# Kernel tuning notes

Hardware: AMD Instinct MI355X
Metric: run time of the kernel (lower is better)

Reference implementation:

```python
import jax, jax.numpy as jnp
import numpy as np

B, L, D, F, E, K = 2, 2048, 1024, 4096, 8, 2


def setup_inputs() -> dict:
    key = jax.random.key(0)
    ks = jax.random.split(key, 8)
    s = 0.02
    return {
        "x": jax.random.normal(ks[0], (B, L, D), dtype=jnp.float32),
        "Wg": jax.random.normal(ks[1], (D, E), dtype=jnp.float32) * s,
        "bg": jnp.zeros((E,), dtype=jnp.float32),
        "W1": jax.random.normal(ks[2], (E, D, F), dtype=jnp.float32) * s,
        "b1": jnp.zeros((E, F), dtype=jnp.float32),
        "W2": jax.random.normal(ks[3], (E, F, D), dtype=jnp.float32) * s,
        "b2": jnp.zeros((E, D), dtype=jnp.float32),
    }


def reference(x, Wg, bg, W1, b1, W2, b2):
    num_experts = Wg.shape[1]
    gate_scores = x @ Wg + bg                                # [B,L,E]
    topk_scores, topk_ids = jax.lax.top_k(gate_scores, K)    # [B,L,K]
    topk_weights = jax.nn.softmax(topk_scores, axis=-1)      # [B,L,K]
    gate_probs = jax.nn.softmax(gate_scores, axis=-1)        # [B,L,E]

    onehot = jax.nn.one_hot(topk_ids, num_experts, dtype=x.dtype)  # [B,L,K,E]
    expert_mask = onehot.sum(axis=2)                         # [B,L,E]
    freq = expert_mask.mean(axis=(0, 1))                     # [E]
    prob_mean = gate_probs.mean(axis=(0, 1))                 # [E]
    load_balance_loss = num_experts * jnp.sum(freq * prob_mean)

    # combine weight per token per expert (0 if expert not selected)
    combine = jnp.sum(onehot * topk_weights[..., None], axis=2)    # [B,L,E]

    # dense dispatch: run every expert FFN on all tokens, weight & combine
    h = jnp.einsum('bld,edf->belf', x, W1) + b1[None, :, None, :]  # [B,E,L,F]
    h = jax.nn.gelu(h, approximate=False)                          # exact GELU (torch default)
    y = jnp.einsum('belf,efd->beld', h, W2) + b2[None, :, None, :] # [B,E,L,D]
    out = jnp.einsum('ble,beld->bld', combine, y)                  # [B,L,D]
    return out, load_balance_loss
```

## Files before the change

kernel.cpp:

```cpp
#include <hip/hip_runtime.h>
#include <hip/hip_bf16.h>
#include <cstdint>
#include <cstddef>

#define B_ 2
#define L_ 2048
#define D_ 1024
#define F_ 4096
#define E_ 8
#define NTOK 4096
#define MAXROWS 9216

typedef __hip_bfloat16 bf16;
typedef __attribute__((ext_vector_type(8))) short short8;
typedef __attribute__((ext_vector_type(4))) float floatx4;

typedef const __attribute__((address_space(1))) uint32_t* gptr_t;
typedef __attribute__((address_space(3))) uint32_t* lptr_t;

__device__ __forceinline__ void async_load16(const bf16* gp, bf16* lp) {
    __builtin_amdgcn_global_load_lds((gptr_t)(const void*)gp, (lptr_t)(void*)lp, 16, 0, 0);
}

__device__ __forceinline__ uint16_t bfbits(bf16 h) {
    union { bf16 b; uint16_t u; } v; v.b = h; return v.u;
}
__device__ __forceinline__ uint32_t pack2(float a, float b) {
    return (uint32_t)bfbits(__float2bfloat16(a)) | ((uint32_t)bfbits(__float2bfloat16(b)) << 16);
}
__device__ __forceinline__ float ublo(uint32_t u){ return __uint_as_float(u << 16); }
__device__ __forceinline__ float ubhi(uint32_t u){ return __uint_as_float(u & 0xffff0000u); }

__global__ __launch_bounds__(256) void gate_kernel(
    const float* __restrict__ x, const float* __restrict__ Wg,
    const float* __restrict__ bg, float* __restrict__ psum_pad,
    uint32_t* __restrict__ top_ids, float* __restrict__ top_w)
{
    __shared__ float psum_l[E_];
    int t = threadIdx.x;
    if (t < E_) psum_l[t] = 0.f;
    __syncthreads();

    int wave = t >> 6, lane = t & 63;
    for (int j = 0; j < 4; ++j) {
        int token = blockIdx.x * 16 + wave * 4 + j;
        const float* xr = x + (size_t)token * D_;

        float acc[E_];
#pragma unroll
        for (int e = 0; e < E_; ++e) acc[e] = 0.f;
        for (int i = 0; i < D_/64; ++i) {
            int d = lane + 64*i;
            float xv = xr[d];
            const float4* wr4 = (const float4*)(Wg + (size_t)d * E_);
            float4 wa = wr4[0], wb = wr4[1];
            acc[0] += xv * wa.x;  acc[1] += xv * wa.y;
            acc[2] += xv * wa.z;  acc[3] += xv * wa.w;
            acc[4] += xv * wb.x;  acc[5] += xv * wb.y;
            acc[6] += xv * wb.z;  acc[7] += xv * wb.w;
        }
#pragma unroll
        for (int off = 32; off >= 1; off >>= 1) {
#pragma unroll
            for (int e = 0; e < E_; ++e) acc[e] += __shfl_xor(acc[e], off, 64);
        }
        if (lane == 0) {
            float s[E_];
#pragma unroll
            for (int e = 0; e < E_; ++e) s[e] = acc[e] + bg[e];
            int i0 = 0;
#pragma unroll
            for (int e = 1; e < E_; ++e) if (s[e] > s[i0]) i0 = e;
            int i1 = -1;
#pragma unroll
            for (int e = 0; e < E_; ++e) {
                if (e == i0) continue;
                if (i1 < 0 || s[e] > s[i1]) i1 = e;
            }
            float e1 = expf(s[i1] - s[i0]);
            float w0 = 1.f / (1.f + e1);
            float w1 = e1 * w0;
            top_ids[token] = (uint32_t)i0 | ((uint32_t)i1 << 8);
            top_w[token]        = w0;
            top_w[NTOK + token] = w1;

            float mx = s[i0], p[E_], sum = 0.f;
#pragma unroll
            for (int e = 0; e < E_; ++e) { p[e] = expf(s[e] - mx); sum += p[e]; }
            float inv = 1.f / sum;
#pragma unroll
            for (int e = 0; e < E_; ++e) atomicAdd(&psum_l[e], p[e] * inv);
        }
    }
    __syncthreads();
    if (t < E_) atomicAdd(&psum_pad[t * 32], psum_l[t]);
}

__global__ __launch_bounds__(256) void compact_kernel(
    const uint32_t* __restrict__ top_ids, const float* __restrict__ top_w,
    int* __restrict__ cnt, int* __restrict__ tok_list, float* __restrict__ w_list,
    int* __restrict__ rowid)
{
    int e = blockIdx.x;
    int t = threadIdx.x, wave = t >> 6, lane = t & 63;
    __shared__ int wcnt[4];
    int base = 0;
    for (int r0 = 0; r0 < NTOK; r0 += 256) {
        int token = r0 + t;
        uint32_t ids = top_ids[token];
        int slot = -1;
        if ((int)(ids & 255u) == e) slot = 0;
        else if ((int)((ids >> 8) & 255u) == e) slot = 1;
        unsigned long long mask = __ballot(slot >= 0);
        int lpos = __popcll(mask & ((1ull << lane) - 1ull));
        if (lane == 0) wcnt[wave] = (int)__popcll(mask);
        __syncthreads();
        int woff = 0, tot = 0;
#pragma unroll
        for (int w2 = 0; w2 < 4; ++w2) { if (w2 < wave) woff += wcnt[w2]; tot += wcnt[w2]; }
        if (slot >= 0) {
            int pos = base + woff + lpos;
            tok_list[e*NTOK + pos] = token;
            w_list[e*NTOK + pos]   = top_w[slot*NTOK + token];
            rowid[slot*NTOK + token] = (e << 13) | pos;
        }
        base += tot;
        __syncthreads();
    }
    if (t == 0) cnt[e] = base;
}

__global__ void finalize_gate_kernel(const int* __restrict__ cnt, const float* __restrict__ psum_pad,
                                     int* __restrict__ off, float* __restrict__ loss_out)
{
    int o = 0; float Ls = 0.f;
    for (int e = 0; e < E_; ++e) {
        off[e] = o;
        o += (cnt[e] + 127) & ~127;
        Ls += (float)cnt[e] * psum_pad[e * 32];
    }
    loss_out[0] = (float)E_ * Ls / ((float)NTOK * (float)NTOK);
}

__global__ __launch_bounds__(256) void transpose_bf16_kernel(
    const float* __restrict__ in, bf16* __restrict__ outp, int R, int C)
{
    int tilesR = R >> 7, tilesC = C >> 6;
    int per = tilesR * tilesC;
    int bx = blockIdx.x;
    int e  = bx / per; int r2 = bx % per;
    int tr = r2 / tilesC, tc = r2 % tilesC;
    int r0 = tr << 7, c0 = tc << 6;
    const float* ip = in  + (size_t)e * R * C;
    bf16*        op = outp + (size_t)e * R * C;

    int t = threadIdx.x;
    int c = (t & 15) * 4;
    int r = (t >> 4) * 8;

    const float* p = ip + (size_t)(r0 + r) * C + c0 + c;
    float4 v[8];
#pragma unroll
    for (int j = 0; j < 8; ++j) v[j] = *(const float4*)(p + (size_t)j * C);
    const float* vf = (const float*)v;

#pragma unroll
    for (int i = 0; i < 4; ++i) {
        uint4 o;
        o.x = pack2(vf[0*4+i], vf[1*4+i]);
        o.y = pack2(vf[2*4+i], vf[3*4+i]);
        o.z = pack2(vf[4*4+i], vf[5*4+i]);
        o.w = pack2(vf[6*4+i], vf[7*4+i]);
        *(uint4*)(op + (size_t)(c0 + c + i) * R + r0 + r) = o;
    }
}

__global__ __launch_bounds__(256) void gather_kernel(
    const float* __restrict__ x, const int* __restrict__ cnt, const int* __restrict__ off,
    const int* __restrict__ tok_list, bf16* __restrict__ Xg)
{
    int bx = blockIdx.x;
    int e  = bx >> 12;
    int i  = bx & 4095;
    if (i >= cnt[e]) return;
    int tok = tok_list[e*NTOK + i];
    size_t row = (size_t)(off[e] + i);
    int t = threadIdx.x;
    float4 v = *(const float4*)(x + (size_t)tok * D_ + t*4);
    uint2 uu;
    uu.x = pack2(v.x, v.y);
    uu.y = pack2(v.z, v.w);
    *(uint2*)(Xg + row * D_ + t*4) = uu;
}

__global__ __launch_bounds__(256) void gemm1_kernel(
    const bf16* __restrict__ Xg, const bf16* __restrict__ W1t,
    const float* __restrict__ b1, const int* __restrict__ cnt,
    const int* __restrict__ off, bf16* __restrict__ H)
{
    int bx = blockIdx.x;
    int e  = bx >> 10;
    int r2 = bx & 1023;
    int mtile = r2 >> 5, ntile = r2 & 31;
    int n = cnt[e];
    if (mtile * 128 >= n) return;
    int row0 = off[e] + mtile * 128;
    int f0 = ntile * 128;

    __shared__ bf16 As[128*64];
    __shared__ bf16 Bs[128*64];

    int t = threadIdx.x;
    int wave = t >> 6, lane = t & 63;
    int wm = wave & 1, wn = wave >> 1;
    int q = lane >> 4, ln = lane & 15;
    int sm = lane >> 3, sc = lane & 7;

    const bf16* Abase = Xg  + (size_t)row0 * D_;
    const bf16* Bbase = W1t + ((size_t)e * F_ + f0) * D_;

    floatx4 acc[4][4];
#pragma unroll
    for (int mt = 0; mt < 4; ++mt)
#pragma unroll
        for (int nt = 0; nt < 4; ++nt) acc[mt][nt] = {0.f, 0.f, 0.f, 0.f};

    for (int kt = 0; kt < D_; kt += 64) {
        __syncthreads();
#pragma unroll
        for (int i = 0; i < 4; ++i) {
            int g = wave*4 + i;
            int m = g*8 + sm;
            int ca = sc ^ (m & 7);
            async_load16(Abase + (size_t)m * D_ + kt + ca*8, &As[g*512]);
            async_load16(Bbase + (size_t)m * D_ + kt + ca*8, &Bs[g*512]);
        }
        __syncthreads();
#pragma unroll
        for (int kk = 0; kk < 2; ++kk) {
            short8 av[4], bv[4];
#pragma unroll
            for (int mt = 0; mt < 4; ++mt) {
                int r = wm*64 + mt*16 + ln;
                int cs = (kk*4 + q) ^ (r & 7);
                av[mt] = *(const short8*)&As[r*64 + cs*8];
            }
#pragma unroll
            for (int nt = 0; nt < 4; ++nt) {
                int r = wn*64 + nt*16 + ln;
                int cs = (kk*4 + q) ^ (r & 7);
                bv[nt] = *(const short8*)&Bs[r*64 + cs*8];
            }
#pragma unroll
            for (int mt = 0; mt < 4; ++mt)
#pragma unroll
                for (int nt = 0; nt < 4; ++nt)
                    acc[mt][nt] = __builtin_amdgcn_mfma_f32_16x16x32_bf16(av[mt], bv[nt], acc[mt][nt], 0, 0, 0);
        }
    }

    const float is2 = 0.70710678118654752f;
#pragma unroll
    for (int nt = 0; nt < 4; ++nt) {
        int f = f0 + wn*64 + nt*16 + ln;
        float b1v = b1[(size_t)e * F_ + f];
#pragma unroll
        for (int mt = 0; mt < 4; ++mt) {
            int rl = wm*64 + mt*16 + q*4;
#pragma unroll
            for (int r = 0; r < 4; ++r) {
                float v = acc[mt][nt][r] + b1v;
                v = 0.5f * v * (1.f + erff(v * is2));
                H[(size_t)(row0 + rl + r) * F_ + f] = __float2bfloat16(v);
            }
        }
    }
}

__global__ __launch_bounds__(256) void gemm2_kernel(
    const bf16* __restrict__ H, const bf16* __restrict__ W2t,
    const float* __restrict__ b2, const int* __restrict__ cnt, const int* __restrict__ off,
    bf16* __restrict__ Y)
{
    int bx = blockIdx.x;
    int e   = bx >> 8;
    int rem = bx & 255;
    int mtile = rem >> 3;
    int ntile = rem & 7;
    int n = cnt[e];
    if (mtile * 128 >= n) return;
    int row0 = off[e] + mtile * 128;
    int d0 = ntile * 128;

    __shared__ bf16 As[128*64];
    __shared__ bf16 Bs[128*64];

    int t = threadIdx.x;
    int wave = t >> 6, lane = t & 63;
    int wm = wave & 1, wn = wave >> 1;
    int q = lane >> 4, ln = lane & 15;
    int sm = lane >> 3, sc = lane & 7;

    const bf16* Abase = H   + (size_t)row0 * F_;
    const bf16* Bbase = W2t + ((size_t)e * D_ + d0) * F_;

    floatx4 acc[4][4];
#pragma unroll
    for (int mt = 0; mt < 4; ++mt)
#pragma unroll
        for (int nt = 0; nt < 4; ++nt) acc[mt][nt] = {0.f, 0.f, 0.f, 0.f};

    for (int kt = 0; kt < F_; kt += 64) {
        __syncthreads();
#pragma unroll
        for (int i = 0; i < 4; ++i) {
            int g = wave*4 + i;
            int m = g*8 + sm;
            int ca = sc ^ (m & 7);
            async_load16(Abase + (size_t)m * F_ + kt + ca*8, &As[g*512]);
            async_load16(Bbase + (size_t)m * F_ + kt + ca*8, &Bs[g*512]);
        }
        __syncthreads();
#pragma unroll
        for (int kk = 0; kk < 2; ++kk) {
            short8 av[4], bv[4];
#pragma unroll
            for (int mt = 0; mt < 4; ++mt) {
                int r = wm*64 + mt*16 + ln;
                int cs = (kk*4 + q) ^ (r & 7);
                av[mt] = *(const short8*)&As[r*64 + cs*8];
            }
#pragma unroll
            for (int nt = 0; nt < 4; ++nt) {
                int r = wn*64 + nt*16 + ln;
                int cs = (kk*4 + q) ^ (r & 7);
                bv[nt] = *(const short8*)&Bs[r*64 + cs*8];
            }
#pragma unroll
            for (int mt = 0; mt < 4; ++mt)
#pragma unroll
                for (int nt = 0; nt < 4; ++nt)
                    acc[mt][nt] = __builtin_amdgcn_mfma_f32_16x16x32_bf16(av[mt], bv[nt], acc[mt][nt], 0, 0, 0);
        }
    }

    float b2v[4];
#pragma unroll
    for (int nt = 0; nt < 4; ++nt)
        b2v[nt] = b2[(size_t)e * D_ + d0 + wn*64 + nt*16 + ln];

#pragma unroll
    for (int mt = 0; mt < 4; ++mt) {
#pragma unroll
        for (int r = 0; r < 4; ++r) {
            int loc = wm*64 + mt*16 + q*4 + r;
            int i = mtile*128 + loc;
            if (i < n) {
                bf16* yp = Y + (size_t)(row0 + loc) * D_ + d0;
#pragma unroll
                for (int nt = 0; nt < 4; ++nt)
                    yp[wn*64 + nt*16 + ln] = __float2bfloat16(acc[mt][nt][r] + b2v[nt]);
            }
        }
    }
}

__global__ __launch_bounds__(256) void combine_kernel(
    const bf16* __restrict__ Y, const int* __restrict__ rowid,
    const float* __restrict__ top_w, const int* __restrict__ off,
    float* __restrict__ out)
{
    int tok = blockIdx.x;
    int t = threadIdx.x;
    int v0 = rowid[tok], v1 = rowid[NTOK + tok];
    float w0 = top_w[tok], w1 = top_w[NTOK + tok];
    size_t r0 = (size_t)(off[v0 >> 13] + (v0 & 8191));
    size_t r1 = (size_t)(off[v1 >> 13] + (v1 & 8191));
    uint2 a = *(const uint2*)(Y + r0 * D_ + t*4);
    uint2 b = *(const uint2*)(Y + r1 * D_ + t*4);
    float4 o;
    o.x = w0 * ublo(a.x) + w1 * ublo(b.x);
    o.y = w0 * ubhi(a.x) + w1 * ubhi(b.x);
    o.z = w0 * ublo(a.y) + w1 * ublo(b.y);
    o.w = w0 * ubhi(a.y) + w1 * ubhi(b.y);
    *(float4*)(out + (size_t)tok * D_ + t*4) = o;
}

extern "C" void kernel_launch(void* const* d_in, const int* in_sizes, int n_in,
                              void* d_out, int out_size, void* d_ws, size_t ws_size,
                              hipStream_t stream)
{
    const float* x  = (const float*)d_in[0];
    const float* Wg = (const float*)d_in[1];
    const float* bg = (const float*)d_in[2];
    const float* W1 = (const float*)d_in[3];
    const float* b1 = (const float*)d_in[4];
    const float* W2 = (const float*)d_in[5];
    const float* b2 = (const float*)d_in[6];
    float* out = (float*)d_out;

    char* ws = (char*)d_ws;
    int*      cnt      = (int*)(ws + 0);
    int*      off      = (int*)(ws + 128);
    float*    psum_pad = (float*)(ws + 1024);
    uint32_t* top_ids  = (uint32_t*)(ws + 8192);
    float*    top_w    = (float*)(ws + 8192 + 16384);
    int*      tok_list = (int*)(ws + 65536);
    float*    w_list   = (float*)(ws + 65536 + 131072);
    int*      rowid    = (int*)(ws + 327680);
    size_t o = 1u << 20;
    bf16*  W1t = (bf16*)(ws + o);  o += (size_t)E_ * D_ * F_ * 2;
    bf16*  W2t = (bf16*)(ws + o);  o += (size_t)E_ * F_ * D_ * 2;
    bf16*  Xg  = (bf16*)(ws + o);  o += (size_t)MAXROWS * D_ * 2;
    bf16*  H   = (bf16*)(ws + o);
    bf16*  Y   = Xg;

    hipMemsetAsync(ws + 1024, 0, 1024, stream);

    transpose_bf16_kernel<<<E_ * 8 * 64, 256, 0, stream>>>(W1, W1t, D_, F_);
    transpose_bf16_kernel<<<E_ * 32 * 16, 256, 0, stream>>>(W2, W2t, F_, D_);

    gate_kernel<<<256, 256, 0, stream>>>(x, Wg, bg, psum_pad, top_ids, top_w);
    compact_kernel<<<E_, 256, 0, stream>>>(top_ids, top_w, cnt, tok_list, w_list, rowid);
    finalize_gate_kernel<<<1, 1, 0, stream>>>(cnt, psum_pad, off, out + (size_t)NTOK * D_);
    gather_kernel<<<E_ * 4096, 256, 0, stream>>>(x, cnt, off, tok_list, Xg);

    gemm1_kernel<<<E_ * 32 * 32, 256, 0, stream>>>(Xg, W1t, b1, cnt, off, H);
    gemm2_kernel<<<E_ * 32 * 8, 256, 0, stream>>>(H, W2t, b2, cnt, off, Y);
    combine_kernel<<<NTOK, 256, 0, stream>>>(Y, rowid, top_w, off, out);
}
```

Measured before the change: 684.6 us.

## Stage weight transpose through LDS, vectorize gate loads, use fast GELU

```diff
diff --git a/kernel.cpp b/kernel.cpp
--- a/kernel.cpp
+++ b/kernel.cpp
@@ -31,6 +31,14 @@
 __device__ __forceinline__ float ublo(uint32_t u){ return __uint_as_float(u << 16); }
 __device__ __forceinline__ float ubhi(uint32_t u){ return __uint_as_float(u & 0xffff0000u); }
 
+__device__ __forceinline__ float fast_gelu(float x) {
+    float x2 = x * x;
+    float z = x * fmaf(0.1029432f, x2, 2.3022081f);
+    z = fminf(z, 120.f);
+    float u = __builtin_amdgcn_exp2f(z);
+    return x * u * __builtin_amdgcn_rcpf(1.f + u);
+}
+
 __global__ __launch_bounds__(256) void gate_kernel(
     const float* __restrict__ x, const float* __restrict__ Wg,
     const float* __restrict__ bg, float* __restrict__ psum_pad,
@@ -49,15 +57,21 @@
         float acc[E_];
 #pragma unroll
         for (int e = 0; e < E_; ++e) acc[e] = 0.f;
-        for (int i = 0; i < D_/64; ++i) {
-            int d = lane + 64*i;
-            float xv = xr[d];
-            const float4* wr4 = (const float4*)(Wg + (size_t)d * E_);
-            float4 wa = wr4[0], wb = wr4[1];
-            acc[0] += xv * wa.x;  acc[1] += xv * wa.y;
-            acc[2] += xv * wa.z;  acc[3] += xv * wa.w;
-            acc[4] += xv * wb.x;  acc[5] += xv * wb.y;
-            acc[6] += xv * wb.z;  acc[7] += xv * wb.w;
+#pragma unroll
+        for (int i = 0; i < 4; ++i) {
+            int d = lane * 4 + 256 * i;
+            float4 xv = *(const float4*)(xr + d);
+            const float* xs = &xv.x;
+#pragma unroll
+            for (int jj = 0; jj < 4; ++jj) {
+                const float4* wr4 = (const float4*)(Wg + (size_t)(d + jj) * E_);
+                float4 wa = wr4[0], wb = wr4[1];
+                float xvj = xs[jj];
+                acc[0] += xvj * wa.x;  acc[1] += xvj * wa.y;
+                acc[2] += xvj * wa.z;  acc[3] += xvj * wa.w;
+                acc[4] += xvj * wb.x;  acc[5] += xvj * wb.y;
+                acc[6] += xvj * wb.z;  acc[7] += xvj * wb.w;
+            }
         }
 #pragma unroll
         for (int off = 32; off >= 1; off >>= 1) {
@@ -145,33 +159,40 @@
 __global__ __launch_bounds__(256) void transpose_bf16_kernel(
     const float* __restrict__ in, bf16* __restrict__ outp, int R, int C)
 {
-    int tilesR = R >> 7, tilesC = C >> 6;
+    int tilesR = R >> 6, tilesC = C >> 6;
     int per = tilesR * tilesC;
     int bx = blockIdx.x;
     int e  = bx / per; int r2 = bx % per;
     int tr = r2 / tilesC, tc = r2 % tilesC;
-    int r0 = tr << 7, c0 = tc << 6;
+    int r0 = tr << 6, c0 = tc << 6;
     const float* ip = in  + (size_t)e * R * C;
     bf16*        op = outp + (size_t)e * R * C;
 
-    int t = threadIdx.x;
-    int c = (t & 15) * 4;
-    int r = (t >> 4) * 8;
-
-    const float* p = ip + (size_t)(r0 + r) * C + c0 + c;
-    float4 v[8];
-#pragma unroll
-    for (int j = 0; j < 8; ++j) v[j] = *(const float4*)(p + (size_t)j * C);
-    const float* vf = (const float*)v;
-
-#pragma unroll
-    for (int i = 0; i < 4; ++i) {
-        uint4 o;
-        o.x = pack2(vf[0*4+i], vf[1*4+i]);
-        o.y = pack2(vf[2*4+i], vf[3*4+i]);
-        o.z = pack2(vf[4*4+i], vf[5*4+i]);
-        o.w = pack2(vf[6*4+i], vf[7*4+i]);
-        *(uint4*)(op + (size_t)(c0 + c + i) * R + r0 + r) = o;
+    __shared__ uint32_t T[64][36];
+    int t = threadIdx.x;
+    int rp = t >> 4;
+    int c4 = (t & 15) * 4;
+
+#pragma unroll
+    for (int it = 0; it < 2; ++it) {
+        int pr = rp + 16 * it;
+        const float* p = ip + (size_t)(r0 + 2*pr) * C + c0 + c4;
+        float4 a = *(const float4*)(p);
+        float4 b = *(const float4*)(p + C);
+        T[c4+0][pr] = pack2(a.x, b.x);
+        T[c4+1][pr] = pack2(a.y, b.y);
+        T[c4+2][pr] = pack2(a.z, b.z);
+        T[c4+3][pr] = pack2(a.w, b.w);
+    }
+    __syncthreads();
+
+    int s     = t & 7;
+    int cbase = t >> 3;
+#pragma unroll
+    for (int pass = 0; pass < 2; ++pass) {
+        int cc = cbase + 32 * pass;
+        uint4 u = *(const uint4*)&T[cc][4*s];
+        *(uint4*)(op + (size_t)(c0 + cc) * R + r0 + 8*s) = u;
     }
 }
 
@@ -259,7 +280,6 @@
         }
     }
 
-    const float is2 = 0.70710678118654752f;
 #pragma unroll
     for (int nt = 0; nt < 4; ++nt) {
         int f = f0 + wn*64 + nt*16 + ln;
@@ -270,8 +290,7 @@
 #pragma unroll
             for (int r = 0; r < 4; ++r) {
                 float v = acc[mt][nt][r] + b1v;
-                v = 0.5f * v * (1.f + erff(v * is2));
-                H[(size_t)(row0 + rl + r) * F_ + f] = __float2bfloat16(v);
+                H[(size_t)(row0 + rl + r) * F_ + f] = __float2bfloat16(fast_gelu(v));
             }
         }
     }
@@ -417,8 +436,8 @@
 
     hipMemsetAsync(ws + 1024, 0, 1024, stream);
 
-    transpose_bf16_kernel<<<E_ * 8 * 64, 256, 0, stream>>>(W1, W1t, D_, F_);
-    transpose_bf16_kernel<<<E_ * 32 * 16, 256, 0, stream>>>(W2, W2t, F_, D_);
+    transpose_bf16_kernel<<<E_ * 16 * 64, 256, 0, stream>>>(W1, W1t, D_, F_);
+    transpose_bf16_kernel<<<E_ * 64 * 16, 256, 0, stream>>>(W2, W2t, F_, D_);
 
     gate_kernel<<<256, 256, 0, stream>>>(x, Wg, bg, psum_pad, top_ids, top_w);
     compact_kernel<<<E_, 256, 0, stream>>>(top_ids, top_w, cnt, tok_list, w_list, rowid);
```

Measured after the change: 659.9 us. -3.6%, faster.
